# Kernel optimization log

Hardware: AMD Instinct MI355X
Metric: run time of the kernel (lower is better)

## Reference

```python
import jax, jax.numpy as jnp
import numpy as np

B, L1, L2, DIM_HID = 32, 64, 64, 256
FEAT = 2 * DIM_HID  # per-sequence feature dim; pair dim = 4*dim_hid


def setup_inputs() -> dict:
    key = jax.random.key(0)
    k1, k2, k3, k4, k5, k6 = jax.random.split(key, 6)
    x1 = jax.random.normal(k1, (B, L1, FEAT), dtype=jnp.float32)
    x2 = jax.random.normal(k2, (B, L2, FEAT), dtype=jnp.float32)
    # lengths in [1, L]; force max length so torch's dynamic max_len == L1*L2
    seq_lens1 = jax.random.randint(k3, (B,), 1, L1 + 1).at[0].set(L1)
    seq_lens2 = jax.random.randint(k4, (B,), 1, L2 + 1).at[0].set(L2)
    W = jax.random.normal(k5, (DIM_HID, 4 * DIM_HID), dtype=jnp.float32) * (1.0 / np.sqrt(4 * DIM_HID))
    b = jax.random.normal(k6, (DIM_HID,), dtype=jnp.float32) * 0.01
    return {"x1": x1, "seq_lens1": seq_lens1, "x2": x2, "seq_lens2": seq_lens2, "W": W, "b": b}


def reference(x1, seq_lens1, x2, seq_lens2, W, b):
    # Faithful to torch: for each sample, all (i,j) pairs with i<sl1, j<sl2 get
    # feature concat(x1[i], x2[j]); remaining rows (up to max_len = L1*L2) are
    # zero-padded BEFORE Linear+ReLU, so they contribute relu(b) to the sum.
    # Linear on concat == split GEMM: x1 @ W[:, :F].T + x2 @ W[:, F:].T + b,
    # which avoids materializing the [B, L1*L2, 4h] pair tensor.
    y1 = jnp.einsum('bif,hf->bih', x1, W[:, :FEAT])  # [B, L1, H]
    y2 = jnp.einsum('bjf,hf->bjh', x2, W[:, FEAT:])  # [B, L2, H]
    mask = (jnp.arange(L1)[None, :] < seq_lens1[:, None])[:, :, None] & \
           (jnp.arange(L2)[None, :] < seq_lens2[:, None])[:, None, :]  # [B, L1, L2]
    z = jnp.where(mask[..., None], y1[:, :, None, :] + y2[:, None, :, :] + b, b)
    y = jax.nn.relu(z)  # [B, L1, L2, H]; dropout is identity (eval / p handled)
    denom = (seq_lens1 * seq_lens2).astype(x1.dtype)[:, None]
    return y.sum(axis=(1, 2)) / denom
```

## Files before the change

kernel.cpp:

```cpp
#include <hip/hip_runtime.h>

#define BB 32
#define LL 64
#define HH 256
#define FF 512
#define WSTRIDE 1024
#define MROWS 4096

typedef float float4v __attribute__((ext_vector_type(4)));
typedef short short8  __attribute__((ext_vector_type(8)));

static __device__ __forceinline__ unsigned short f2bf(float x) {
    union { float f; unsigned int u; } v; v.f = x;
    v.u += 0x7FFFu + ((v.u >> 16) & 1u);
    return (unsigned short)(v.u >> 16);
}

__global__ void init_out_kernel(const int* __restrict__ s1,
                                const int* __restrict__ s2,
                                const float* __restrict__ bias,
                                float* __restrict__ out) {
    const int b = blockIdx.x;
    const int h = threadIdx.x;
    const float denom = (float)s1[b] * (float)s2[b];
    const float pad = (float)(LL * LL) - denom;
    out[b * HH + h] = pad * fmaxf(bias[h], 0.0f) / denom;
}

#define BK 64
#define LDS_STRIDE 72
__global__ __launch_bounds__(256)
void gemm_mfma_kernel(const float* __restrict__ x1,
                      const float* __restrict__ x2,
                      const float* __restrict__ W,
                      const float* __restrict__ bias,
                      float* __restrict__ y) {
    const int colBase = blockIdx.x * 64;
    const int rowBase = blockIdx.y * 64;
    const bool second = (rowBase >= 2048);
    const float* __restrict__ A = second ? x2 : x1;
    const int arow0 = second ? (rowBase - 2048) : rowBase;
    const int woff  = second ? FF : 0;

    __shared__ __align__(16) unsigned short As[64][LDS_STRIDE];
    __shared__ __align__(16) unsigned short Bs[64][LDS_STRIDE];

    const int t    = threadIdx.x;
    const int lane = t & 63;
    const int wid  = t >> 6;
    const int wm   = wid >> 1;
    const int wn   = wid & 1;
    const int lm   = lane & 15;
    const int quad = lane >> 4;

    const int r  = t >> 2;
    const int kq = t & 3;

    const float* aPtr = A + (size_t)(arow0 + r) * FF + kq * 16;
    const float* bPtr = W + (size_t)(colBase + r) * WSTRIDE + woff + kq * 16;

    float4v acc[2][2];
    #pragma unroll
    for (int i = 0; i < 2; ++i)
        #pragma unroll
        for (int j = 0; j < 2; ++j)
            acc[i][j] = (float4v){0.f, 0.f, 0.f, 0.f};

    float4 pa[4], pb[4];
    #pragma unroll
    for (int q = 0; q < 4; ++q) {
        pa[q] = *(const float4*)(aPtr + q * 4);
        pb[q] = *(const float4*)(bPtr + q * 4);
    }

    const unsigned short* aB0 = &As[wm * 32 + lm][quad * 8];
    const unsigned short* aB1 = &As[wm * 32 + 16 + lm][quad * 8];
    const unsigned short* bB0 = &Bs[wn * 32 + lm][quad * 8];
    const unsigned short* bB1 = &Bs[wn * 32 + 16 + lm][quad * 8];

    for (int kt = 0; kt < FF / BK; ++kt) {
        short8 wa0, wa1, wb0, wb1;
        {
            const float* fa = (const float*)pa;
            const float* fb = (const float*)pb;
            #pragma unroll
            for (int e = 0; e < 8; ++e) {
                ((unsigned short*)&wa0)[e] = f2bf(fa[e]);
                ((unsigned short*)&wa1)[e] = f2bf(fa[e + 8]);
                ((unsigned short*)&wb0)[e] = f2bf(fb[e]);
                ((unsigned short*)&wb1)[e] = f2bf(fb[e + 8]);
            }
        }
        *(short8*)&As[r][kq * 16]     = wa0;
        *(short8*)&As[r][kq * 16 + 8] = wa1;
        *(short8*)&Bs[r][kq * 16]     = wb0;
        *(short8*)&Bs[r][kq * 16 + 8] = wb1;
        __syncthreads();

        if (kt + 1 < FF / BK) {
            const float* aN = aPtr + (kt + 1) * BK;
            const float* bN = bPtr + (kt + 1) * BK;
            #pragma unroll
            for (int q = 0; q < 4; ++q) {
                pa[q] = *(const float4*)(aN + q * 4);
                pb[q] = *(const float4*)(bN + q * 4);
            }
        }

        #pragma unroll
        for (int ks = 0; ks < 2; ++ks) {
            const short8 a0 = *(const short8*)(aB0 + ks * 32);
            const short8 a1 = *(const short8*)(aB1 + ks * 32);
            const short8 b0 = *(const short8*)(bB0 + ks * 32);
            const short8 b1 = *(const short8*)(bB1 + ks * 32);
            acc[0][0] = __builtin_amdgcn_mfma_f32_16x16x32_bf16(a0, b0, acc[0][0], 0, 0, 0);
            acc[0][1] = __builtin_amdgcn_mfma_f32_16x16x32_bf16(a0, b1, acc[0][1], 0, 0, 0);
            acc[1][0] = __builtin_amdgcn_mfma_f32_16x16x32_bf16(a1, b0, acc[1][0], 0, 0, 0);
            acc[1][1] = __builtin_amdgcn_mfma_f32_16x16x32_bf16(a1, b1, acc[1][1], 0, 0, 0);
        }
        __syncthreads();
    }

    #pragma unroll
    for (int im = 0; im < 2; ++im) {
        #pragma unroll
        for (int in = 0; in < 2; ++in) {
            const int col = colBase + wn * 32 + in * 16 + lm;
            const float bv = second ? bias[col] : 0.0f;
            #pragma unroll
            for (int j = 0; j < 4; ++j) {
                const int row = rowBase + wm * 32 + im * 16 + quad * 4 + j;
                y[(size_t)row * HH + col] = acc[im][in][j] + bv;
            }
        }
    }
}

#define ICH 4
__global__ __launch_bounds__(256)
void pair_kernel(const float* __restrict__ y,
                 const int* __restrict__ s1p,
                 const int* __restrict__ s2p,
                 float* __restrict__ out) {
    const int b  = blockIdx.x;
    const int ic = blockIdx.y;
    const int h  = threadIdx.x;
    const int n1 = s1p[b];
    const int n2 = s2p[b];
    const int i0 = ic * ICH;
    if (i0 >= n1) return;

    const float* __restrict__ y1 = y + (size_t)(b * LL) * HH + h;
    const float* __restrict__ y2 = y + (size_t)(2048 + b * LL) * HH + h;

    float r1[ICH];
    #pragma unroll
    for (int ii = 0; ii < ICH; ++ii) {
        const int i = i0 + ii;
        r1[ii] = (i < n1) ? y1[(size_t)i * HH] : -1e30f;
    }

    float a0 = 0.f, a1 = 0.f, a2 = 0.f, a3 = 0.f;
    int j = 0;
    for (; j + 4 <= n2; j += 4) {
        const float v0 = y2[(size_t)(j + 0) * HH];
        const float v1 = y2[(size_t)(j + 1) * HH];
        const float v2 = y2[(size_t)(j + 2) * HH];
        const float v3 = y2[(size_t)(j + 3) * HH];
        a0 += fmaxf(r1[0] + v0, 0.f); a1 += fmaxf(r1[1] + v0, 0.f);
        a2 += fmaxf(r1[2] + v0, 0.f); a3 += fmaxf(r1[3] + v0, 0.f);
        a0 += fmaxf(r1[0] + v1, 0.f); a1 += fmaxf(r1[1] + v1, 0.f);
        a2 += fmaxf(r1[2] + v1, 0.f); a3 += fmaxf(r1[3] + v1, 0.f);
        a0 += fmaxf(r1[0] + v2, 0.f); a1 += fmaxf(r1[1] + v2, 0.f);
        a2 += fmaxf(r1[2] + v2, 0.f); a3 += fmaxf(r1[3] + v2, 0.f);
        a0 += fmaxf(r1[0] + v3, 0.f); a1 += fmaxf(r1[1] + v3, 0.f);
        a2 += fmaxf(r1[2] + v3, 0.f); a3 += fmaxf(r1[3] + v3, 0.f);
    }
    for (; j < n2; ++j) {
        const float v = y2[(size_t)j * HH];
        a0 += fmaxf(r1[0] + v, 0.f); a1 += fmaxf(r1[1] + v, 0.f);
        a2 += fmaxf(r1[2] + v, 0.f); a3 += fmaxf(r1[3] + v, 0.f);
    }

    const float denom = (float)(n1 * n2);
    atomicAdd(&out[b * HH + h], (a0 + a1 + a2 + a3) / denom);
}

extern "C" void kernel_launch(void* const* d_in, const int* in_sizes, int n_in,
                              void* d_out, int out_size, void* d_ws, size_t ws_size,
                              hipStream_t stream) {
    const float* x1 = (const float*)d_in[0];
    const int*   s1 = (const int*)d_in[1];
    const float* x2 = (const float*)d_in[2];
    const int*   s2 = (const int*)d_in[3];
    const float* W  = (const float*)d_in[4];
    const float* b  = (const float*)d_in[5];
    float* out = (float*)d_out;
    float* y   = (float*)d_ws;

    init_out_kernel<<<BB, HH, 0, stream>>>(s1, s2, b, out);
    gemm_mfma_kernel<<<dim3(HH / 64, MROWS / 64), 256, 0, stream>>>(x1, x2, W, b, y);
    pair_kernel<<<dim3(BB, LL / ICH), 256, 0, stream>>>(y, s1, s2, out);
}
```

Baseline: 85.68 us.

## Fuse init, split GEMM and pairwise ReLU-sum into one kernel per batch tile

Replaces the three-kernel pipeline (output init, global GEMM writing y to workspace, pair reduction with atomics) with a single kernel. Each block handles one batch element and a 32-wide hidden slice, computes both y1 and y2 tiles with MFMA into shared memory, then runs the pairwise ReLU sum from LDS and writes the output directly with the padding term folded in. This removes the workspace round trip, two launches and the atomics. The cost is that W slices are reloaded once per batch element and the grid is only 256 blocks with heavier LDS use per block.

```diff
diff --git a/kernel.cpp b/kernel.cpp
--- a/kernel.cpp
+++ b/kernel.cpp
@@ -5,7 +5,10 @@
 #define HH 256
 #define FF 512
 #define WSTRIDE 1024
-#define MROWS 4096
+#define HT 32
+#define BK 64
+#define LSTR 72
+#define YSTR 33
 
 typedef float float4v __attribute__((ext_vector_type(4)));
 typedef short short8  __attribute__((ext_vector_type(8)));
@@ -16,48 +19,61 @@
     return (unsigned short)(v.u >> 16);
 }
 
-__global__ void init_out_kernel(const int* __restrict__ s1,
-                                const int* __restrict__ s2,
-                                const float* __restrict__ bias,
-                                float* __restrict__ out) {
-    const int b = blockIdx.x;
-    const int h = threadIdx.x;
-    const float denom = (float)s1[b] * (float)s2[b];
-    const float pad = (float)(LL * LL) - denom;
-    out[b * HH + h] = pad * fmaxf(bias[h], 0.0f) / denom;
-}
-
-#define BK 64
-#define LDS_STRIDE 72
+static __device__ __forceinline__ void cvt_store16(const float4* p, unsigned short* dst) {
+    const float* f = (const float*)p;
+    short8 lo, hi;
+    #pragma unroll
+    for (int e = 0; e < 8; ++e) {
+        ((unsigned short*)&lo)[e] = f2bf(f[e]);
+        ((unsigned short*)&hi)[e] = f2bf(f[e + 8]);
+    }
+    *(short8*)dst = lo;
+    *(short8*)(dst + 8) = hi;
+}
+
+static __device__ __forceinline__ void cvt_store8(const float4* p, unsigned short* dst) {
+    const float* f = (const float*)p;
+    short8 lo;
+    #pragma unroll
+    for (int e = 0; e < 8; ++e)
+        ((unsigned short*)&lo)[e] = f2bf(f[e]);
+    *(short8*)dst = lo;
+}
+
 __global__ __launch_bounds__(256)
-void gemm_mfma_kernel(const float* __restrict__ x1,
-                      const float* __restrict__ x2,
-                      const float* __restrict__ W,
-                      const float* __restrict__ bias,
-                      float* __restrict__ y) {
-    const int colBase = blockIdx.x * 64;
-    const int rowBase = blockIdx.y * 64;
-    const bool second = (rowBase >= 2048);
-    const float* __restrict__ A = second ? x2 : x1;
-    const int arow0 = second ? (rowBase - 2048) : rowBase;
-    const int woff  = second ? FF : 0;
-
-    __shared__ __align__(16) unsigned short As[64][LDS_STRIDE];
-    __shared__ __align__(16) unsigned short Bs[64][LDS_STRIDE];
-
-    const int t    = threadIdx.x;
-    const int lane = t & 63;
-    const int wid  = t >> 6;
-    const int wm   = wid >> 1;
-    const int wn   = wid & 1;
-    const int lm   = lane & 15;
-    const int quad = lane >> 4;
-
-    const int r  = t >> 2;
-    const int kq = t & 3;
-
-    const float* aPtr = A + (size_t)(arow0 + r) * FF + kq * 16;
-    const float* bPtr = W + (size_t)(colBase + r) * WSTRIDE + woff + kq * 16;
+void fused_kernel(const float* __restrict__ x1,
+                  const int* __restrict__ s1p,
+                  const float* __restrict__ x2,
+                  const int* __restrict__ s2p,
+                  const float* __restrict__ W,
+                  const float* __restrict__ bias,
+                  float* __restrict__ out) {
+    const int b  = blockIdx.x;
+    const int h0 = blockIdx.y * HT;
+
+    __shared__ __align__(16) unsigned short As1[LL][LSTR];
+    __shared__ __align__(16) unsigned short As2[LL][LSTR];
+    __shared__ __align__(16) unsigned short Bs1[HT][LSTR];
+    __shared__ __align__(16) unsigned short Bs2[HT][LSTR];
+    __shared__ float y1t[LL][YSTR];
+    __shared__ float y2t[LL][YSTR];
+    __shared__ float partial[8][YSTR];
+
+    const int t      = threadIdx.x;
+    const int lane   = t & 63;
+    const int wid    = t >> 6;
+    const int srcSel = wid >> 1;
+    const int mrow   = (wid & 1) * 32;
+    const int lm     = lane & 15;
+    const int quad   = lane >> 4;
+
+    const int r   = t >> 2;  const int kq  = t & 3;
+    const int rw  = t >> 3;  const int kq8 = t & 7;
+
+    const float* a1p = x1 + (size_t)(b * LL + r) * FF + kq * 16;
+    const float* a2p = x2 + (size_t)(b * LL + r) * FF + kq * 16;
+    const float* w1p = W + (size_t)(h0 + rw) * WSTRIDE + kq8 * 8;
+    const float* w2p = W + (size_t)(h0 + rw) * WSTRIDE + FF + kq8 * 8;
 
     float4v acc[2][2];
     #pragma unroll
@@ -66,53 +82,52 @@
         for (int j = 0; j < 2; ++j)
             acc[i][j] = (float4v){0.f, 0.f, 0.f, 0.f};
 
-    float4 pa[4], pb[4];
+    float4 pa1[4], pa2[4], pb1[2], pb2[2];
     #pragma unroll
     for (int q = 0; q < 4; ++q) {
-        pa[q] = *(const float4*)(aPtr + q * 4);
-        pb[q] = *(const float4*)(bPtr + q * 4);
-    }
-
-    const unsigned short* aB0 = &As[wm * 32 + lm][quad * 8];
-    const unsigned short* aB1 = &As[wm * 32 + 16 + lm][quad * 8];
-    const unsigned short* bB0 = &Bs[wn * 32 + lm][quad * 8];
-    const unsigned short* bB1 = &Bs[wn * 32 + 16 + lm][quad * 8];
+        pa1[q] = *(const float4*)(a1p + q * 4);
+        pa2[q] = *(const float4*)(a2p + q * 4);
+    }
+    #pragma unroll
+    for (int q = 0; q < 2; ++q) {
+        pb1[q] = *(const float4*)(w1p + q * 4);
+        pb2[q] = *(const float4*)(w2p + q * 4);
+    }
+
+    const unsigned short (*Ap)[LSTR] = srcSel ? As2 : As1;
+    const unsigned short (*Bp)[LSTR] = srcSel ? Bs2 : Bs1;
+    const unsigned short* aF0 = &Ap[mrow + lm][quad * 8];
+    const unsigned short* aF1 = &Ap[mrow + 16 + lm][quad * 8];
+    const unsigned short* bF0 = &Bp[lm][quad * 8];
+    const unsigned short* bF1 = &Bp[16 + lm][quad * 8];
 
     for (int kt = 0; kt < FF / BK; ++kt) {
-        short8 wa0, wa1, wb0, wb1;
-        {
-            const float* fa = (const float*)pa;
-            const float* fb = (const float*)pb;
+        cvt_store16(pa1, &As1[r][kq * 16]);
+        cvt_store16(pa2, &As2[r][kq * 16]);
+        cvt_store8(pb1, &Bs1[rw][kq8 * 8]);
+        cvt_store8(pb2, &Bs2[rw][kq8 * 8]);
+        __syncthreads();
+
+        if (kt + 1 < FF / BK) {
+            const int ko = (kt + 1) * BK;
             #pragma unroll
-            for (int e = 0; e < 8; ++e) {
-                ((unsigned short*)&wa0)[e] = f2bf(fa[e]);
-                ((unsigned short*)&wa1)[e] = f2bf(fa[e + 8]);
-                ((unsigned short*)&wb0)[e] = f2bf(fb[e]);
-                ((unsigned short*)&wb1)[e] = f2bf(fb[e + 8]);
+            for (int q = 0; q < 4; ++q) {
+                pa1[q] = *(const float4*)(a1p + ko + q * 4);
+                pa2[q] = *(const float4*)(a2p + ko + q * 4);
+            }
+            #pragma unroll
+            for (int q = 0; q < 2; ++q) {
+                pb1[q] = *(const float4*)(w1p + ko + q * 4);
+                pb2[q] = *(const float4*)(w2p + ko + q * 4);
             }
         }
-        *(short8*)&As[r][kq * 16]     = wa0;
-        *(short8*)&As[r][kq * 16 + 8] = wa1;
-        *(short8*)&Bs[r][kq * 16]     = wb0;
-        *(short8*)&Bs[r][kq * 16 + 8] = wb1;
-        __syncthreads();
-
-        if (kt + 1 < FF / BK) {
-            const float* aN = aPtr + (kt + 1) * BK;
-            const float* bN = bPtr + (kt + 1) * BK;
-            #pragma unroll
-            for (int q = 0; q < 4; ++q) {
-                pa[q] = *(const float4*)(aN + q * 4);
-                pb[q] = *(const float4*)(bN + q * 4);
-            }
-        }
 
         #pragma unroll
         for (int ks = 0; ks < 2; ++ks) {
-            const short8 a0 = *(const short8*)(aB0 + ks * 32);
-            const short8 a1 = *(const short8*)(aB1 + ks * 32);
-            const short8 b0 = *(const short8*)(bB0 + ks * 32);
-            const short8 b1 = *(const short8*)(bB1 + ks * 32);
+            const short8 a0 = *(const short8*)(aF0 + ks * 32);
+            const short8 a1 = *(const short8*)(aF1 + ks * 32);
+            const short8 b0 = *(const short8*)(bF0 + ks * 32);
+            const short8 b1 = *(const short8*)(bF1 + ks * 32);
             acc[0][0] = __builtin_amdgcn_mfma_f32_16x16x32_bf16(a0, b0, acc[0][0], 0, 0, 0);
             acc[0][1] = __builtin_amdgcn_mfma_f32_16x16x32_bf16(a0, b1, acc[0][1], 0, 0, 0);
             acc[1][0] = __builtin_amdgcn_mfma_f32_16x16x32_bf16(a1, b0, acc[1][0], 0, 0, 0);
@@ -121,69 +136,62 @@
         __syncthreads();
     }
 
-    #pragma unroll
-    for (int im = 0; im < 2; ++im) {
-        #pragma unroll
-        for (int in = 0; in < 2; ++in) {
-            const int col = colBase + wn * 32 + in * 16 + lm;
-            const float bv = second ? bias[col] : 0.0f;
+    {
+        float (*yt)[YSTR] = srcSel ? y2t : y1t;
+        float bv[2];
+        bv[0] = srcSel ? bias[h0 + lm] : 0.0f;
+        bv[1] = srcSel ? bias[h0 + 16 + lm] : 0.0f;
+        #pragma unroll
+        for (int im = 0; im < 2; ++im)
             #pragma unroll
-            for (int j = 0; j < 4; ++j) {
-                const int row = rowBase + wm * 32 + im * 16 + quad * 4 + j;
-                y[(size_t)row * HH + col] = acc[im][in][j] + bv;
-            }
-        }
-    }
-}
-
-#define ICH 4
-__global__ __launch_bounds__(256)
-void pair_kernel(const float* __restrict__ y,
-                 const int* __restrict__ s1p,
-                 const int* __restrict__ s2p,
-                 float* __restrict__ out) {
-    const int b  = blockIdx.x;
-    const int ic = blockIdx.y;
-    const int h  = threadIdx.x;
+            for (int in = 0; in < 2; ++in)
+                #pragma unroll
+                for (int j = 0; j < 4; ++j)
+                    yt[mrow + im * 16 + quad * 4 + j][in * 16 + lm] = acc[im][in][j] + bv[in];
+    }
+    __syncthreads();
+
     const int n1 = s1p[b];
     const int n2 = s2p[b];
-    const int i0 = ic * ICH;
-    if (i0 >= n1) return;
-
-    const float* __restrict__ y1 = y + (size_t)(b * LL) * HH + h;
-    const float* __restrict__ y2 = y + (size_t)(2048 + b * LL) * HH + h;
-
-    float r1[ICH];
-    #pragma unroll
-    for (int ii = 0; ii < ICH; ++ii) {
-        const int i = i0 + ii;
-        r1[ii] = (i < n1) ? y1[(size_t)i * HH] : -1e30f;
-    }
-
-    float a0 = 0.f, a1 = 0.f, a2 = 0.f, a3 = 0.f;
+    const int h  = t & 31;
+    const int ic = t >> 5;
+
+    float r1[8];
+    #pragma unroll
+    for (int ii = 0; ii < 8; ++ii) {
+        const int i = ic * 8 + ii;
+        r1[ii] = (i < n1) ? y1t[i][h] : -1e30f;
+    }
+
+    float ac[8] = {0.f, 0.f, 0.f, 0.f, 0.f, 0.f, 0.f, 0.f};
     int j = 0;
-    for (; j + 4 <= n2; j += 4) {
-        const float v0 = y2[(size_t)(j + 0) * HH];
-        const float v1 = y2[(size_t)(j + 1) * HH];
-        const float v2 = y2[(size_t)(j + 2) * HH];
-        const float v3 = y2[(size_t)(j + 3) * HH];
-        a0 += fmaxf(r1[0] + v0, 0.f); a1 += fmaxf(r1[1] + v0, 0.f);
-        a2 += fmaxf(r1[2] + v0, 0.f); a3 += fmaxf(r1[3] + v0, 0.f);
-        a0 += fmaxf(r1[0] + v1, 0.f); a1 += fmaxf(r1[1] + v1, 0.f);
-        a2 += fmaxf(r1[2] + v1, 0.f); a3 += fmaxf(r1[3] + v1, 0.f);
-        a0 += fmaxf(r1[0] + v2, 0.f); a1 += fmaxf(r1[1] + v2, 0.f);
-        a2 += fmaxf(r1[2] + v2, 0.f); a3 += fmaxf(r1[3] + v2, 0.f);
-        a0 += fmaxf(r1[0] + v3, 0.f); a1 += fmaxf(r1[1] + v3, 0.f);
-        a2 += fmaxf(r1[2] + v3, 0.f); a3 += fmaxf(r1[3] + v3, 0.f);
-    }
-    for (; j < n2; ++j) {
-        const float v = y2[(size_t)j * HH];
-        a0 += fmaxf(r1[0] + v, 0.f); a1 += fmaxf(r1[1] + v, 0.f);
-        a2 += fmaxf(r1[2] + v, 0.f); a3 += fmaxf(r1[3] + v, 0.f);
-    }
-
-    const float denom = (float)(n1 * n2);
-    atomicAdd(&out[b * HH + h], (a0 + a1 + a2 + a3) / denom);
+    for (; j + 2 <= n2; j += 2) {
+        const float v0 = y2t[j][h];
+        const float v1 = y2t[j + 1][h];
+        #pragma unroll
+        for (int ii = 0; ii < 8; ++ii) {
+            ac[ii] += fmaxf(r1[ii] + v0, 0.f);
+            ac[ii] += fmaxf(r1[ii] + v1, 0.f);
+        }
+    }
+    if (j < n2) {
+        const float v0 = y2t[j][h];
+        #pragma unroll
+        for (int ii = 0; ii < 8; ++ii)
+            ac[ii] += fmaxf(r1[ii] + v0, 0.f);
+    }
+    partial[ic][h] = ((ac[0] + ac[1]) + (ac[2] + ac[3])) + ((ac[4] + ac[5]) + (ac[6] + ac[7]));
+    __syncthreads();
+
+    if (t < 32) {
+        float s = 0.f;
+        #pragma unroll
+        for (int ic2 = 0; ic2 < 8; ++ic2)
+            s += partial[ic2][t];
+        const float denom = (float)(n1 * n2);
+        const float pad = (float)(LL * LL) - denom;
+        out[b * HH + h0 + t] = (s + pad * fmaxf(bias[h0 + t], 0.f)) / denom;
+    }
 }
 
 extern "C" void kernel_launch(void* const* d_in, const int* in_sizes, int n_in,
@@ -196,9 +204,6 @@
     const float* W  = (const float*)d_in[4];
     const float* b  = (const float*)d_in[5];
     float* out = (float*)d_out;
-    float* y   = (float*)d_ws;
-
-    init_out_kernel<<<BB, HH, 0, stream>>>(s1, s2, b, out);
-    gemm_mfma_kernel<<<dim3(HH / 64, MROWS / 64), 256, 0, stream>>>(x1, x2, W, b, y);
-    pair_kernel<<<dim3(BB, LL / ICH), 256, 0, stream>>>(y, s1, s2, out);
-}
+
+    fused_kernel<<<dim3(BB, HH / HT), 256, 0, stream>>>(x1, s1, x2, s2, W, b, out);
+}
```

Measured after the change: 78.42 us. -8.5%, faster.
